# Kernel optimization log

Hardware: AMD Instinct MI355X
Metric: run time of the kernel (lower is better)

Reference implementation:

```python
import jax, jax.numpy as jnp
import numpy as np

B, S, D = 2, 2048, 2048
H = 16
HD = D // H  # 128
ROPE_THETA = 10000.0


def _rotate_half(x):
    # interleaved rotate: [-x2_0, x1_0, -x2_1, x1_1, ...]
    x1 = x[..., ::2]
    x2 = x[..., 1::2]
    return jnp.stack((-x2, x1), axis=-1).reshape(x.shape)


def _rope_cos_sin(seq_len, head_dim, dtype):
    inv_freq = 1.0 / (ROPE_THETA ** (jnp.arange(0, head_dim, 2, dtype=jnp.float32) / head_dim))
    pos = jnp.arange(seq_len, dtype=jnp.float32)
    freqs = pos[:, None] * inv_freq[None, :]          # [S, HD/2]
    angles = jnp.concatenate((freqs, freqs), axis=-1)  # [S, HD]  (matches torch.cat((freqs, freqs), -1))
    return jnp.cos(angles).astype(dtype), jnp.sin(angles).astype(dtype)


def setup_inputs() -> dict:
    key = jax.random.key(0)
    ks = jax.random.split(key, 5)
    scale = 1.0 / np.sqrt(D)
    return {
        "x": jax.random.normal(ks[0], (B, S, D), dtype=jnp.float32),
        "Wq": jax.random.normal(ks[1], (D, D), dtype=jnp.float32) * scale,
        "Wk": jax.random.normal(ks[2], (D, D), dtype=jnp.float32) * scale,
        "Wv": jax.random.normal(ks[3], (D, D), dtype=jnp.float32) * scale,
        "Wo": jax.random.normal(ks[4], (D, D), dtype=jnp.float32) * scale,
    }


def reference(x, Wq, Wk, Wv, Wo):
    b, s, d = x.shape
    # separate Q/K/V projections (no bias), reshape to [B, H, S, HD]
    def proj(W):
        return jnp.einsum('bsd,de->bse', x, W).reshape(b, s, H, HD).transpose(0, 2, 1, 3)
    q, k, v = proj(Wq), proj(Wk), proj(Wv)

    cos, sin = _rope_cos_sin(s, HD, q.dtype)  # [S, HD]
    cos = cos[None, None, :, :]
    sin = sin[None, None, :, :]
    q = q * cos + _rotate_half(q) * sin
    k = k * cos + _rotate_half(k) * sin

    # causal scaled dot-product attention
    scores = jnp.einsum('bhqd,bhkd->bhqk', q, k) / jnp.sqrt(jnp.asarray(HD, q.dtype))
    causal = jnp.tril(jnp.ones((s, s), dtype=bool))
    scores = jnp.where(causal[None, None, :, :], scores, jnp.asarray(-jnp.inf, scores.dtype))
    attn = jax.nn.softmax(scores, axis=-1)
    out = jnp.einsum('bhqk,bhkd->bhqd', attn, v)

    out = out.transpose(0, 2, 1, 3).reshape(b, s, d)
    return jnp.einsum('bsd,de->bse', out, Wo)
```

## Files before the change

kernel.cpp:

```cpp
#include <hip/hip_runtime.h>
#include <hip/hip_bf16.h>
#include <math.h>

typedef unsigned short u16;
typedef unsigned int u32;

#define Bz 2
#define Sz 2048
#define Dz 2048
#define Hz 16
#define HDz 128
#define Mz 4096

typedef __bf16 bf16x8 __attribute__((ext_vector_type(8)));
typedef float f32x4 __attribute__((ext_vector_type(4)));

__device__ __forceinline__ float bf2f(u16 h) {
    union { u32 u; float f; } x; x.u = ((u32)h) << 16; return x.f;
}
__device__ __forceinline__ u16 f2bf(float f) {
    union { float f; u32 u; } x; x.f = f;
    u32 u = x.u;
    return (u16)((u + 0x7FFFu + ((u >> 16) & 1u)) >> 16);
}
__device__ __forceinline__ u32 pack_bf16_trunc(float lo, float hi) {
    union { float f; u32 u; } a, b; a.f = lo; b.f = hi;
    return (a.u >> 16) | (b.u & 0xFFFF0000u);
}
__device__ __forceinline__ u32 pack_bf16_rn(float lo, float hi) {
    return (u32)f2bf(lo) | ((u32)f2bf(hi) << 16);
}
__device__ __forceinline__ float fexp2(float x) {
#if __has_builtin(__builtin_amdgcn_exp2f)
    return __builtin_amdgcn_exp2f(x);
#else
    return exp2f(x);
#endif
}
__device__ __forceinline__ void gl_lds16(const void* g, void* l) {
    __builtin_amdgcn_global_load_lds(
        (const __attribute__((address_space(1))) void*)g,
        (__attribute__((address_space(3))) void*)l, 16, 0, 0);
}

__global__ void cvt_f32_bf16(const float* __restrict__ src, u16* __restrict__ dst) {
    size_t i = (size_t)blockIdx.x * blockDim.x + threadIdx.x;
    float4 a = ((const float4*)src)[2 * i];
    float4 b = ((const float4*)src)[2 * i + 1];
    u16 r[8] = {f2bf(a.x), f2bf(a.y), f2bf(a.z), f2bf(a.w),
                f2bf(b.x), f2bf(b.y), f2bf(b.z), f2bf(b.w)};
    *(uint4*)(dst + 8 * i) = *(const uint4*)r;
}

__global__ void transpose_w(const float* __restrict__ W0, const float* __restrict__ W1,
                            const float* __restrict__ W2, const float* __restrict__ W3,
                            u16* __restrict__ Wt) {
    __shared__ u16 t[64][65];
    const float* src = (blockIdx.z == 0) ? W0 : (blockIdx.z == 1) ? W1
                     : (blockIdx.z == 2) ? W2 : W3;
    u16* dst = Wt + (size_t)blockIdx.z * (Dz * Dz);
    int x = blockIdx.x * 64, y = blockIdx.y * 64;
    int c = threadIdx.x & 63, rb = (threadIdx.x >> 6) * 16;
#pragma unroll
    for (int i = 0; i < 16; i++) {
        int r = rb + i;
        t[r][c] = f2bf(src[(size_t)(y + r) * Dz + x + c]);
    }
    __syncthreads();
#pragma unroll
    for (int i = 0; i < 16; i++) {
        int r = rb + i;
        dst[(size_t)(x + r) * Dz + y + c] = t[c][r];
    }
}

template <int MODE>
__global__ void gemm_bt(const u16* __restrict__ A, const u16* __restrict__ BtBase,
                        void* __restrict__ CBase) {
    const int z = blockIdx.z;
    const u16* Bt = BtBase + (size_t)z * (Dz * Dz);
    const int tid = threadIdx.x, lane = tid & 63, wave = tid >> 6;
    const int ln = lane & 15, qd = lane >> 4;
    const int m0 = blockIdx.y * 128, n0 = blockIdx.x * 128;

    __shared__ __align__(16) u16 As[128][64];
    __shared__ __align__(16) u16 Bs[128][64];

    f32x4 acc[4][4];
#pragma unroll
    for (int i = 0; i < 4; i++)
#pragma unroll
        for (int j = 0; j < 4; j++) acc[i][j] = (f32x4){0.f, 0.f, 0.f, 0.f};

    const int wm = (wave >> 1) * 64, wn = (wave & 1) * 64;
    const int lr8 = lane >> 3;
    const int bgo = (((lane & 7) ^ lr8) * 8);
    const int x7 = ln & 7;

    for (int k0 = 0; k0 < Dz; k0 += 64) {
        const u16* ga = A  + (size_t)(m0 + wave * 32 + lr8) * Dz + k0 + bgo;
        const u16* gb = Bt + (size_t)(n0 + wave * 32 + lr8) * Dz + k0 + bgo;
#pragma unroll
        for (int i = 0; i < 4; i++) {
            gl_lds16(ga + (size_t)(8 * i) * Dz, &As[wave * 32 + 8 * i][0]);
            gl_lds16(gb + (size_t)(8 * i) * Dz, &Bs[wave * 32 + 8 * i][0]);
        }
        __syncthreads();
#pragma unroll
        for (int kc = 0; kc < 2; kc++) {
            bf16x8 af[4], bff[4];
            const int cs = ((4 * kc + qd) ^ x7) * 8;
#pragma unroll
            for (int i = 0; i < 4; i++) {
                af[i]  = *(const bf16x8*)&As[wm + i * 16 + ln][cs];
                bff[i] = *(const bf16x8*)&Bs[wn + i * 16 + ln][cs];
            }
#pragma unroll
            for (int i = 0; i < 4; i++)
#pragma unroll
                for (int j = 0; j < 4; j++)
                    acc[i][j] = __builtin_amdgcn_mfma_f32_16x16x32_bf16(
                        af[i], bff[j], acc[i][j], 0, 0, 0);
        }
        __syncthreads();
    }

#pragma unroll
    for (int i = 0; i < 4; i++) {
#pragma unroll
        for (int j = 0; j < 4; j++) {
#pragma unroll
            for (int r = 0; r < 4; r++) {
                int row = m0 + wm + i * 16 + qd * 4 + r;
                int col = n0 + wn + j * 16 + ln;
                if (MODE == 0) {
                    ((float*)CBase)[(size_t)row * Dz + col] = acc[i][j][r];
                } else {
                    u16* C = (u16*)CBase + (size_t)z * ((size_t)Mz * Dz);
                    u16 hv = f2bf(acc[i][j][r]);
                    int bb = row >> 11, ss = row & 2047;
                    int hh = col >> 7, hd = col & 127;
                    if (z == 2)
                        C[((size_t)(bb * Hz + hh) * HDz + hd) * Sz + ss] = hv;
                    else
                        C[((size_t)(bb * Hz + hh) * Sz + ss) * HDz + hd] = hv;
                }
            }
        }
    }
}

__global__ void rope_kernel(u16* __restrict__ Q, u16* __restrict__ Kk) {
    u32 idx = blockIdx.x * blockDim.x + threadIdx.x;
    int isK = (idx >> 22) & 1;
    u16* T = isK ? Kk : Q;
    u32 p = idx & 0x3FFFFFu;
    int j = p & 63;
    int s = (p >> 6) & 2047;
    size_t base = (size_t)(p >> 6) * HDz + 2 * j;
    u32 u = *(u32*)(T + base);
    float x0 = bf2f((u16)(u & 0xFFFFu));
    float x1 = bf2f((u16)(u >> 16));
    int i0 = (2 * j) & 63;
    const float LG = 0.20762050593046017f;
    float f0 = exp2f(-LG * (float)i0);
    float f1 = exp2f(-LG * (float)(i0 + 1));
    float th0 = (float)s * f0, th1 = (float)s * f1;
    float s0, c0, s1, c1;
    sincosf(th0, &s0, &c0);
    sincosf(th1, &s1, &c1);
    float scl = isK ? 1.0f : 0.12751771218027603f;
    float y0 = (x0 * c0 - x1 * s0) * scl;
    float y1 = (x1 * c1 + x0 * s1) * scl;
    u32 outw = (u32)f2bf(y0) | ((u32)f2bf(y1) << 16);
    *(u32*)(T + base) = outw;
}

__global__ __launch_bounds__(256, 4)
void flash_attn(const u16* __restrict__ Q, const u16* __restrict__ Kk,
                const u16* __restrict__ Vt, u16* __restrict__ O) {
    const int tid = threadIdx.x, lane = tid & 63, wave = tid >> 6;
    const int ln = lane & 15, qd = lane >> 4;
    const int bh = blockIdx.x & 31;
    const int qt = 31 - (blockIdx.x >> 5);
    const int b = bh >> 4, h = bh & 15;
    const int q0 = qt * 64;
    const u16* Qh = Q  + (size_t)bh * Sz * HDz;
    const u16* Kh = Kk + (size_t)bh * Sz * HDz;
    const u16* Vh = Vt + (size_t)bh * HDz * Sz;

    __shared__ __align__(16) u16 Ks[64][128];
    __shared__ __align__(16) u16 Vs[144][64];

    for (int idx = tid; idx < 16 * 64; idx += 256) {
        int rr = idx >> 6, cc = idx & 63;
        Vs[128 + rr][cc] = (rr == 0) ? (u16)0x3F80 : (u16)0;
    }

    const int qabs = q0 + wave * 16 + ln;
    bf16x8 qf[4];
#pragma unroll
    for (int kc = 0; kc < 4; kc++) {
        uint4 t = *(const uint4*)(Qh + (size_t)qabs * HDz + kc * 32 + qd * 8);
        qf[kc] = *(const bf16x8*)&t;
    }

    float m_run = -INFINITY;
    f32x4 oa[9];
#pragma unroll
    for (int n = 0; n < 9; n++) oa[n] = (f32x4){0.f, 0.f, 0.f, 0.f};

    const int x7 = ln & 7;
    const int l4 = lane >> 4, c16 = lane & 15;
    const int lr8 = lane >> 3;
    const int bgv = ((lane & 7) ^ lr8) * 8;

    for (int k0 = 0; k0 <= q0; k0 += 64) {
        {
#pragma unroll
            for (int i = 0; i < 4; i++) {
                int rw = 4 * (i & 1) + l4;
                const u16* gk = Kh + (size_t)(k0 + 16 * wave + 4 * i + l4) * HDz
                                   + ((c16 ^ rw) * 8);
                gl_lds16(gk, &Ks[16 * wave + 4 * i][0]);
            }
            const u16* gv = Vh + (size_t)(32 * wave + lr8) * Sz + k0 + bgv;
#pragma unroll
            for (int i = 0; i < 4; i++)
                gl_lds16(gv + (size_t)(8 * i) * Sz, &Vs[32 * wave + 8 * i][0]);
        }
        __syncthreads();

        f32x4 sc4[4];
#pragma unroll
        for (int mt = 0; mt < 4; mt++) sc4[mt] = (f32x4){0.f, 0.f, 0.f, 0.f};
#pragma unroll
        for (int kc = 0; kc < 4; kc++) {
            const int cs = ((4 * kc + qd) ^ x7) * 8;
#pragma unroll
            for (int mt = 0; mt < 4; mt++) {
                bf16x8 kf = *(const bf16x8*)&Ks[mt * 16 + ln][cs];
                sc4[mt] = __builtin_amdgcn_mfma_f32_16x16x32_bf16(kf, qf[kc], sc4[mt], 0, 0, 0);
            }
        }
        if (k0 == q0) {
#pragma unroll
            for (int mt = 0; mt < 4; mt++)
#pragma unroll
                for (int r = 0; r < 4; r++)
                    if (mt * 16 + qd * 4 + r > 16 * wave + ln) sc4[mt][r] = -3e38f;
        }

        float rm = -3e38f;
#pragma unroll
        for (int mt = 0; mt < 4; mt++) {
            rm = fmaxf(rm, fmaxf(fmaxf(sc4[mt][0], sc4[mt][1]),
                                 fmaxf(sc4[mt][2], sc4[mt][3])));
        }
        rm = fmaxf(rm, __shfl_xor(rm, 16));
        rm = fmaxf(rm, __shfl_xor(rm, 32));
        float mn = fmaxf(m_run, rm);
        bool resc = (__ballot(mn > m_run) != 0ULL);
        float al = fexp2(m_run - mn);
        m_run = mn;
        if (resc) {
#pragma unroll
            for (int n = 0; n < 9; n++)
#pragma unroll
                for (int r = 0; r < 4; r++) oa[n][r] *= al;
        }

        u32 pku[8];
#pragma unroll
        for (int mt = 0; mt < 4; mt++) {
#pragma unroll
            for (int t = 0; t < 2; t++)
                pku[mt * 2 + t] = pack_bf16_trunc(fexp2(sc4[mt][2 * t] - mn),
                                                  fexp2(sc4[mt][2 * t + 1] - mn));
        }

#pragma unroll
        for (int kc = 0; kc < 2; kc++) {
            union { u32 w[4]; bf16x8 v; } pb;
#pragma unroll
            for (int s = 0; s < 4; s++) {
                int srcl = ((2 * (qd & 1) + (s >> 1)) << 4) | ln;
                u32 a0 = (u32)__shfl((int)pku[4 * kc + (s & 1)], srcl);
                u32 a1 = (u32)__shfl((int)pku[4 * kc + 2 + (s & 1)], srcl);
                pb.w[s] = (qd & 2) ? a1 : a0;
            }
            const int cs = ((4 * kc + qd) ^ x7) * 8;
#pragma unroll
            for (int mt = 0; mt < 9; mt++) {
                bf16x8 vf = *(const bf16x8*)&Vs[mt * 16 + ln][cs];
                oa[mt] = __builtin_amdgcn_mfma_f32_16x16x32_bf16(vf, pb.v, oa[mt], 0, 0, 0);
            }
        }
        __syncthreads();
    }

    float l = __shfl(oa[8][0], ln);
    float linv = 1.0f / l;
    u16* op = O + ((size_t)b * Sz + qabs) * Dz + h * HDz;
#pragma unroll
    for (int mt = 0; mt < 8; mt++) {
        u32 w0 = pack_bf16_rn(oa[mt][0] * linv, oa[mt][1] * linv);
        u32 w1 = pack_bf16_rn(oa[mt][2] * linv, oa[mt][3] * linv);
        uint2 ww; ww.x = w0; ww.y = w1;
        *(uint2*)(op + mt * 16 + qd * 4) = ww;
    }
}

extern "C" void kernel_launch(void* const* d_in, const int* in_sizes, int n_in,
                              void* d_out, int out_size, void* d_ws, size_t ws_size,
                              hipStream_t stream) {
    const float* x  = (const float*)d_in[0];
    const float* Wq = (const float*)d_in[1];
    const float* Wk = (const float*)d_in[2];
    const float* Wv = (const float*)d_in[3];
    const float* Wo = (const float*)d_in[4];
    u16* ws  = (u16*)d_ws;

    u16* wt = ws;
    u16* q  = ws + 16777216;
    u16* kk = q + 8388608;
    u16* v  = kk + 8388608;
    u16* xb = v + 8388608;
    u16* o  = xb;

    cvt_f32_bf16<<<dim3(4096), 256, 0, stream>>>(x, xb);
    transpose_w<<<dim3(32, 32, 4), 256, 0, stream>>>(Wq, Wk, Wv, Wo, wt);
    gemm_bt<1><<<dim3(16, 32, 3), 256, 0, stream>>>(xb, wt, q);
    rope_kernel<<<dim3(32768), 256, 0, stream>>>(q, kk);
    flash_attn<<<dim3(1024), 256, 0, stream>>>(q, kk, v, o);
    gemm_bt<0><<<dim3(16, 32, 1), 256, 0, stream>>>(o, wt + 3 * 4194304, (float*)d_out);
}
```

Baseline: 397.5 us.

## Double query rows per wave in flash attention to reuse K/V tiles

The flash attention kernel now gives each wave 32 query rows (two 16-row groups) and each block 128 queries, so every K/V tile in LDS feeds twice as many MFMAs. The grid is halved and launch bounds relaxed to allow more registers. The row-sum trick that appended a ones-row to V is replaced by an explicit running l computed with shuffles. The block schedule is also interleaved to balance causal work. Costs are higher register pressure, lower occupancy and some idle waves on diagonal tiles.

```diff
diff --git a/kernel.cpp b/kernel.cpp
--- a/kernel.cpp
+++ b/kernel.cpp
@@ -176,46 +176,49 @@
     *(u32*)(T + base) = outw;
 }
 
-__global__ __launch_bounds__(256, 4)
+__global__ __launch_bounds__(256, 2)
 void flash_attn(const u16* __restrict__ Q, const u16* __restrict__ Kk,
                 const u16* __restrict__ Vt, u16* __restrict__ O) {
     const int tid = threadIdx.x, lane = tid & 63, wave = tid >> 6;
     const int ln = lane & 15, qd = lane >> 4;
     const int bh = blockIdx.x & 31;
-    const int qt = 31 - (blockIdx.x >> 5);
+    const int g = blockIdx.x >> 5;
+    const int qt = (g < 8) ? (15 - g) : (g - 8);
     const int b = bh >> 4, h = bh & 15;
-    const int q0 = qt * 64;
+    const int q0 = qt * 128;
+    const int qw0 = q0 + 32 * wave;
     const u16* Qh = Q  + (size_t)bh * Sz * HDz;
     const u16* Kh = Kk + (size_t)bh * Sz * HDz;
     const u16* Vh = Vt + (size_t)bh * HDz * Sz;
 
     __shared__ __align__(16) u16 Ks[64][128];
-    __shared__ __align__(16) u16 Vs[144][64];
-
-    for (int idx = tid; idx < 16 * 64; idx += 256) {
-        int rr = idx >> 6, cc = idx & 63;
-        Vs[128 + rr][cc] = (rr == 0) ? (u16)0x3F80 : (u16)0;
-    }
-
-    const int qabs = q0 + wave * 16 + ln;
-    bf16x8 qf[4];
-#pragma unroll
-    for (int kc = 0; kc < 4; kc++) {
-        uint4 t = *(const uint4*)(Qh + (size_t)qabs * HDz + kc * 32 + qd * 8);
-        qf[kc] = *(const bf16x8*)&t;
-    }
-
-    float m_run = -INFINITY;
-    f32x4 oa[9];
-#pragma unroll
-    for (int n = 0; n < 9; n++) oa[n] = (f32x4){0.f, 0.f, 0.f, 0.f};
+    __shared__ __align__(16) u16 Vs[128][64];
+
+    bf16x8 qf[2][4];
+#pragma unroll
+    for (int g2 = 0; g2 < 2; g2++)
+#pragma unroll
+        for (int kc = 0; kc < 4; kc++) {
+            uint4 t = *(const uint4*)(Qh + (size_t)(qw0 + 16 * g2 + ln) * HDz
+                                      + kc * 32 + qd * 8);
+            qf[g2][kc] = *(const bf16x8*)&t;
+        }
+
+    float m_run[2] = {-INFINITY, -INFINITY};
+    float l_run[2] = {0.f, 0.f};
+    f32x4 oa[2][8];
+#pragma unroll
+    for (int g2 = 0; g2 < 2; g2++)
+#pragma unroll
+        for (int n = 0; n < 8; n++) oa[g2][n] = (f32x4){0.f, 0.f, 0.f, 0.f};
 
     const int x7 = ln & 7;
     const int l4 = lane >> 4, c16 = lane & 15;
     const int lr8 = lane >> 3;
     const int bgv = ((lane & 7) ^ lr8) * 8;
 
-    for (int k0 = 0; k0 <= q0; k0 += 64) {
+    const int kmax = q0 + 64;
+    for (int k0 = 0; k0 <= kmax; k0 += 64) {
         {
 #pragma unroll
             for (int i = 0; i < 4; i++) {
@@ -231,83 +234,111 @@
         }
         __syncthreads();
 
-        f32x4 sc4[4];
-#pragma unroll
-        for (int mt = 0; mt < 4; mt++) sc4[mt] = (f32x4){0.f, 0.f, 0.f, 0.f};
-#pragma unroll
-        for (int kc = 0; kc < 4; kc++) {
-            const int cs = ((4 * kc + qd) ^ x7) * 8;
-#pragma unroll
-            for (int mt = 0; mt < 4; mt++) {
-                bf16x8 kf = *(const bf16x8*)&Ks[mt * 16 + ln][cs];
-                sc4[mt] = __builtin_amdgcn_mfma_f32_16x16x32_bf16(kf, qf[kc], sc4[mt], 0, 0, 0);
-            }
-        }
-        if (k0 == q0) {
-#pragma unroll
-            for (int mt = 0; mt < 4; mt++)
-#pragma unroll
-                for (int r = 0; r < 4; r++)
-                    if (mt * 16 + qd * 4 + r > 16 * wave + ln) sc4[mt][r] = -3e38f;
-        }
-
-        float rm = -3e38f;
-#pragma unroll
-        for (int mt = 0; mt < 4; mt++) {
-            rm = fmaxf(rm, fmaxf(fmaxf(sc4[mt][0], sc4[mt][1]),
-                                 fmaxf(sc4[mt][2], sc4[mt][3])));
-        }
-        rm = fmaxf(rm, __shfl_xor(rm, 16));
-        rm = fmaxf(rm, __shfl_xor(rm, 32));
-        float mn = fmaxf(m_run, rm);
-        bool resc = (__ballot(mn > m_run) != 0ULL);
-        float al = fexp2(m_run - mn);
-        m_run = mn;
-        if (resc) {
-#pragma unroll
-            for (int n = 0; n < 9; n++)
-#pragma unroll
-                for (int r = 0; r < 4; r++) oa[n][r] *= al;
-        }
-
-        u32 pku[8];
-#pragma unroll
-        for (int mt = 0; mt < 4; mt++) {
-#pragma unroll
-            for (int t = 0; t < 2; t++)
-                pku[mt * 2 + t] = pack_bf16_trunc(fexp2(sc4[mt][2 * t] - mn),
-                                                  fexp2(sc4[mt][2 * t + 1] - mn));
-        }
-
-#pragma unroll
-        for (int kc = 0; kc < 2; kc++) {
-            union { u32 w[4]; bf16x8 v; } pb;
-#pragma unroll
-            for (int s = 0; s < 4; s++) {
-                int srcl = ((2 * (qd & 1) + (s >> 1)) << 4) | ln;
-                u32 a0 = (u32)__shfl((int)pku[4 * kc + (s & 1)], srcl);
-                u32 a1 = (u32)__shfl((int)pku[4 * kc + 2 + (s & 1)], srcl);
-                pb.w[s] = (qd & 2) ? a1 : a0;
-            }
-            const int cs = ((4 * kc + qd) ^ x7) * 8;
-#pragma unroll
-            for (int mt = 0; mt < 9; mt++) {
-                bf16x8 vf = *(const bf16x8*)&Vs[mt * 16 + ln][cs];
-                oa[mt] = __builtin_amdgcn_mfma_f32_16x16x32_bf16(vf, pb.v, oa[mt], 0, 0, 0);
+        if (k0 <= qw0 + 31) {
+            f32x4 sc[2][4];
+#pragma unroll
+            for (int g2 = 0; g2 < 2; g2++)
+#pragma unroll
+                for (int mt = 0; mt < 4; mt++) sc[g2][mt] = (f32x4){0.f, 0.f, 0.f, 0.f};
+#pragma unroll
+            for (int kc = 0; kc < 4; kc++) {
+                const int cs = ((4 * kc + qd) ^ x7) * 8;
+#pragma unroll
+                for (int mt = 0; mt < 4; mt++) {
+                    bf16x8 kf = *(const bf16x8*)&Ks[mt * 16 + ln][cs];
+                    sc[0][mt] = __builtin_amdgcn_mfma_f32_16x16x32_bf16(kf, qf[0][kc], sc[0][mt], 0, 0, 0);
+                    sc[1][mt] = __builtin_amdgcn_mfma_f32_16x16x32_bf16(kf, qf[1][kc], sc[1][mt], 0, 0, 0);
+                }
+            }
+            if (k0 + 63 > qw0) {
+#pragma unroll
+                for (int g2 = 0; g2 < 2; g2++) {
+                    int qq = qw0 + 16 * g2 + ln;
+#pragma unroll
+                    for (int mt = 0; mt < 4; mt++)
+#pragma unroll
+                        for (int r = 0; r < 4; r++)
+                            if (k0 + mt * 16 + qd * 4 + r > qq) sc[g2][mt][r] = -3e38f;
+                }
+            }
+
+            u32 pku[2][8];
+#pragma unroll
+            for (int g2 = 0; g2 < 2; g2++) {
+                float rm = -3e38f;
+#pragma unroll
+                for (int mt = 0; mt < 4; mt++)
+                    rm = fmaxf(rm, fmaxf(fmaxf(sc[g2][mt][0], sc[g2][mt][1]),
+                                         fmaxf(sc[g2][mt][2], sc[g2][mt][3])));
+                rm = fmaxf(rm, __shfl_xor(rm, 16));
+                rm = fmaxf(rm, __shfl_xor(rm, 32));
+                float mn = fmaxf(m_run[g2], rm);
+                bool resc = (__ballot(mn > m_run[g2]) != 0ULL);
+                float al = fexp2(m_run[g2] - mn);
+                m_run[g2] = mn;
+                if (resc) {
+                    l_run[g2] *= al;
+#pragma unroll
+                    for (int n = 0; n < 8; n++)
+#pragma unroll
+                        for (int r = 0; r < 4; r++) oa[g2][n][r] *= al;
+                }
+                float sum = 0.f;
+#pragma unroll
+                for (int mt = 0; mt < 4; mt++)
+#pragma unroll
+                    for (int r = 0; r < 4; r++) {
+                        float p = fexp2(sc[g2][mt][r] - mn);
+                        sc[g2][mt][r] = p;
+                        sum += p;
+                    }
+                sum += __shfl_xor(sum, 16);
+                sum += __shfl_xor(sum, 32);
+                l_run[g2] += sum;
+#pragma unroll
+                for (int mt = 0; mt < 4; mt++)
+#pragma unroll
+                    for (int t = 0; t < 2; t++)
+                        pku[g2][mt * 2 + t] =
+                            pack_bf16_trunc(sc[g2][mt][2 * t], sc[g2][mt][2 * t + 1]);
+            }
+
+#pragma unroll
+            for (int kc = 0; kc < 2; kc++) {
+                union { u32 w[4]; bf16x8 v; } pb[2];
+#pragma unroll
+                for (int g2 = 0; g2 < 2; g2++)
+#pragma unroll
+                    for (int s = 0; s < 4; s++) {
+                        int srcl = ((2 * (qd & 1) + (s >> 1)) << 4) | ln;
+                        u32 a0 = (u32)__shfl((int)pku[g2][4 * kc + (s & 1)], srcl);
+                        u32 a1 = (u32)__shfl((int)pku[g2][4 * kc + 2 + (s & 1)], srcl);
+                        pb[g2].w[s] = (qd & 2) ? a1 : a0;
+                    }
+                const int cs = ((4 * kc + qd) ^ x7) * 8;
+#pragma unroll
+                for (int mt = 0; mt < 8; mt++) {
+                    bf16x8 vf = *(const bf16x8*)&Vs[mt * 16 + ln][cs];
+                    oa[0][mt] = __builtin_amdgcn_mfma_f32_16x16x32_bf16(vf, pb[0].v, oa[0][mt], 0, 0, 0);
+                    oa[1][mt] = __builtin_amdgcn_mfma_f32_16x16x32_bf16(vf, pb[1].v, oa[1][mt], 0, 0, 0);
+                }
             }
         }
         __syncthreads();
     }
 
-    float l = __shfl(oa[8][0], ln);
-    float linv = 1.0f / l;
-    u16* op = O + ((size_t)b * Sz + qabs) * Dz + h * HDz;
-#pragma unroll
-    for (int mt = 0; mt < 8; mt++) {
-        u32 w0 = pack_bf16_rn(oa[mt][0] * linv, oa[mt][1] * linv);
-        u32 w1 = pack_bf16_rn(oa[mt][2] * linv, oa[mt][3] * linv);
-        uint2 ww; ww.x = w0; ww.y = w1;
-        *(uint2*)(op + mt * 16 + qd * 4) = ww;
+#pragma unroll
+    for (int g2 = 0; g2 < 2; g2++) {
+        float linv = 1.0f / l_run[g2];
+        int qq = qw0 + 16 * g2 + ln;
+        u16* op = O + ((size_t)b * Sz + qq) * Dz + h * HDz;
+#pragma unroll
+        for (int mt = 0; mt < 8; mt++) {
+            u32 w0 = pack_bf16_rn(oa[g2][mt][0] * linv, oa[g2][mt][1] * linv);
+            u32 w1 = pack_bf16_rn(oa[g2][mt][2] * linv, oa[g2][mt][3] * linv);
+            uint2 ww; ww.x = w0; ww.y = w1;
+            *(uint2*)(op + mt * 16 + qd * 4) = ww;
+        }
     }
 }
 
@@ -332,6 +363,6 @@
     transpose_w<<<dim3(32, 32, 4), 256, 0, stream>>>(Wq, Wk, Wv, Wo, wt);
     gemm_bt<1><<<dim3(16, 32, 3), 256, 0, stream>>>(xb, wt, q);
     rope_kernel<<<dim3(32768), 256, 0, stream>>>(q, kk);
-    flash_attn<<<dim3(1024), 256, 0, stream>>>(q, kk, v, o);
+    flash_attn<<<dim3(512), 256, 0, stream>>>(q, kk, v, o);
     gemm_bt<0><<<dim3(16, 32, 1), 256, 0, stream>>>(o, wt + 3 * 4194304, (float*)d_out);
 }
```

After: 406.9 us. 1.02x slower.
